# Kernel tuning notes

Hardware: AMD Instinct MI355X
Metric: run time of the kernel (lower is better)

Reference implementation:

```python
import jax, jax.numpy as jnp
import numpy as np

D, NH, DH, DM = 1024, 16, 64, 4096
B, S = 2, 2048
EPS = 1e-5


def _layernorm(x, w, b):
    mu = jnp.mean(x, axis=-1, keepdims=True)
    var = jnp.mean((x - mu) ** 2, axis=-1, keepdims=True)
    return (x - mu) * jax.lax.rsqrt(var + EPS) * w + b


def setup_inputs() -> dict:
    key = jax.random.key(0)
    ks = jax.random.split(key, 8)
    scale = D ** (-0.5)
    x = jax.random.normal(ks[0], (B, S, D), dtype=jnp.float32)
    WQ = jax.random.normal(ks[1], (NH, D, DH), dtype=jnp.float32) * scale
    WK = jax.random.normal(ks[2], (NH, D, DH), dtype=jnp.float32) * scale
    WV = jax.random.normal(ks[3], (NH, D, DH), dtype=jnp.float32) * scale
    WO = jax.random.normal(ks[4], (NH, DH, D), dtype=jnp.float32) * scale
    # MLP: torch Linear default init ~ U(-1/sqrt(fan_in), 1/sqrt(fan_in)); stored as [in, out]
    W1 = jax.random.uniform(ks[5], (D, DM), dtype=jnp.float32, minval=-1.0, maxval=1.0) * D ** (-0.5)
    b1 = jnp.zeros((DM,), dtype=jnp.float32)
    W2 = jax.random.uniform(ks[6], (DM, D), dtype=jnp.float32, minval=-1.0, maxval=1.0) * DM ** (-0.5)
    b2 = jnp.zeros((D,), dtype=jnp.float32)
    ln1_w = jnp.ones((D,), dtype=jnp.float32)
    ln1_b = jnp.zeros((D,), dtype=jnp.float32)
    ln2_w = jnp.ones((D,), dtype=jnp.float32)
    ln2_b = jnp.zeros((D,), dtype=jnp.float32)
    return {"x": x, "WQ": WQ, "WK": WK, "WV": WV, "WO": WO,
            "W1": W1, "b1": b1, "W2": W2, "b2": b2,
            "ln1_w": ln1_w, "ln1_b": ln1_b, "ln2_w": ln2_w, "ln2_b": ln2_b}


def reference(x, WQ, WK, WV, WO, W1, b1, W2, b2, ln1_w, ln1_b, ln2_w, ln2_b):
    s = x.shape[1]
    dh = WQ.shape[-1]
    r = x
    h = _layernorm(x, ln1_w, ln1_b)
    # batched across all heads (original loops over h; math identical)
    Q = jnp.einsum('bsd,hde->bhse', h, WQ)
    K = jnp.einsum('bsd,hde->bhse', h, WK)
    V = jnp.einsum('bsd,hde->bhse', h, WV)
    scores = jnp.einsum('bhqe,bhke->bhqk', Q, K) / jnp.sqrt(jnp.float32(dh))
    causal = jnp.tril(jnp.ones((s, s), dtype=bool))  # True = keep
    scores = jnp.where(causal, scores, -jnp.inf)
    attn = jax.nn.softmax(scores, axis=-1)
    ctx = jnp.einsum('bhqk,bhke->bhqe', attn, V)
    ao = jnp.einsum('bhqe,hed->bqd', ctx, WO)  # sum over heads
    x = r + ao
    h2 = _layernorm(x, ln2_w, ln2_b)
    mlp = jax.nn.gelu(h2 @ W1 + b1, approximate=False) @ W2 + b2
    return x + mlp
```

## Files before the change

kernel.cpp:

```cpp
#include <hip/hip_runtime.h>
#include <hip/hip_bf16.h>
#include <cstdint>

#define D_MODEL 1024
#define NHEADS 16
#define DHEAD 64
#define DMLP 4096
#define BATCH 2
#define SEQ 2048
#define ROWS (BATCH*SEQ)
#define LN_EPS 1e-5f

typedef __attribute__((ext_vector_type(8))) short short8;
typedef __attribute__((ext_vector_type(4))) float f32x4;

typedef const __attribute__((address_space(1))) uint32_t* gas_ptr;
typedef __attribute__((address_space(3))) uint32_t* las_ptr;

__device__ __forceinline__ short f2bf(float f) {
  union { float f; uint32_t u; } v; v.f = f;
  uint32_t r = v.u + 0x7FFFu + ((v.u >> 16) & 1u);
  return (short)(r >> 16);
}
__device__ __forceinline__ float bf2f(short s) {
  union { uint32_t u; float f; } v; v.u = ((uint32_t)(uint16_t)s) << 16;
  return v.f;
}

__global__ void ln_kernel(const float* __restrict__ x, const float* __restrict__ w,
                          const float* __restrict__ b, short* __restrict__ out) {
  int row = blockIdx.x;
  int t = threadIdx.x;
  const float4 v = ((const float4*)(x + (size_t)row * D_MODEL))[t];
  float s = v.x + v.y + v.z + v.w;
  float s2 = v.x*v.x + v.y*v.y + v.z*v.z + v.w*v.w;
#pragma unroll
  for (int k = 1; k < 64; k <<= 1) { s += __shfl_xor(s, k); s2 += __shfl_xor(s2, k); }
  __shared__ float red[8];
  int wv = t >> 6;
  if ((t & 63) == 0) { red[wv] = s; red[wv + 4] = s2; }
  __syncthreads();
  s = red[0] + red[1] + red[2] + red[3];
  s2 = red[4] + red[5] + red[6] + red[7];
  float mu = s * (1.0f / D_MODEL);
  float var = s2 * (1.0f / D_MODEL) - mu * mu;
  float rstd = rsqrtf(var + LN_EPS);
  const float4 wv4 = ((const float4*)w)[t];
  const float4 bv4 = ((const float4*)b)[t];
  short4 o4;
  o4.x = f2bf((v.x - mu) * rstd * wv4.x + bv4.x);
  o4.y = f2bf((v.y - mu) * rstd * wv4.y + bv4.y);
  o4.z = f2bf((v.z - mu) * rstd * wv4.z + bv4.z);
  o4.w = f2bf((v.w - mu) * rstd * wv4.w + bv4.w);
  *(short4*)(out + (size_t)row * D_MODEL + t * 4) = o4;
}

__global__ void reduce_ln(float* __restrict__ out, const float* __restrict__ part,
                          const float* __restrict__ w, const float* __restrict__ b,
                          short* __restrict__ h2) {
  int row = blockIdx.x;
  int t = threadIdx.x;
  float4 v = ((float4*)(out + (size_t)row * D_MODEL))[t];
  const float4 q = ((const float4*)(part + (size_t)row * D_MODEL))[t];
  v.x += q.x; v.y += q.y; v.z += q.z; v.w += q.w;
  ((float4*)(out + (size_t)row * D_MODEL))[t] = v;
  float s = v.x + v.y + v.z + v.w;
  float s2 = v.x*v.x + v.y*v.y + v.z*v.z + v.w*v.w;
#pragma unroll
  for (int k = 1; k < 64; k <<= 1) { s += __shfl_xor(s, k); s2 += __shfl_xor(s2, k); }
  __shared__ float red[8];
  int wv = t >> 6;
  if ((t & 63) == 0) { red[wv] = s; red[wv + 4] = s2; }
  __syncthreads();
  s = red[0] + red[1] + red[2] + red[3];
  s2 = red[4] + red[5] + red[6] + red[7];
  float mu = s * (1.0f / D_MODEL);
  float var = s2 * (1.0f / D_MODEL) - mu * mu;
  float rstd = rsqrtf(var + LN_EPS);
  const float4 wv4 = ((const float4*)w)[t];
  const float4 bv4 = ((const float4*)b)[t];
  short4 o4;
  o4.x = f2bf((v.x - mu) * rstd * wv4.x + bv4.x);
  o4.y = f2bf((v.y - mu) * rstd * wv4.y + bv4.y);
  o4.z = f2bf((v.z - mu) * rstd * wv4.z + bv4.z);
  o4.w = f2bf((v.w - mu) * rstd * wv4.w + bv4.w);
  *(short4*)(h2 + (size_t)row * D_MODEL + t * 4) = o4;
}

__global__ __launch_bounds__(256) void repack_w(const float* __restrict__ W, short* __restrict__ out,
                                                int nkt, int ks1, int ks2, int ns1, int ns2) {
  const int cp = blockIdx.x, kt = blockIdx.y;
  const int t = threadIdx.x;
  const int cc = t & 127;
  const int kh = t >> 7;
  const int n = cp * 128 + cc;
  const int nbase = (n >> 6) * ns1 + (n & 63) * ns2;
  short* dst = out + (((size_t)cp * nkt + kt) * 128 + cc) * 64;
#pragma unroll
  for (int ci = 0; ci < 4; ci++) {
    const int c = kh * 4 + ci;
    short8 ch;
#pragma unroll
    for (int j = 0; j < 8; j++) {
      int k = kt * 64 + c * 8 + j;
      ch[j] = f2bf(W[(k >> 6) * ks1 + (k & 63) * ks2 + nbase]);
    }
    const int sp = c ^ (cc & 7);
    *(short8*)(dst + sp * 8) = ch;
  }
}

template<int EPI>
__global__ __launch_bounds__(256) void gemm_bt(const short* __restrict__ A, const short* __restrict__ Bpk,
    const float* __restrict__ bias, const float* __restrict__ resid,
    float* __restrict__ outf, short* __restrict__ outb, float* __restrict__ part,
    int M, int N, int K, int LDA, int KFULL) {
  __shared__ alignas(16) short As[2][8192];
  __shared__ alignas(16) short Bs[2][8192];
  const int t = threadIdx.x;
  const int l = t & 63, w = t >> 6;
  const int l15 = l & 15, l4 = l >> 4;

  const int nx = gridDim.x;
  const int sw = nx >> 3;
  int dd = blockIdx.y * nx + blockIdx.x;
  const int xcd = dd & 7, li = dd >> 3;
  const int bx = xcd * sw + (li % sw);
  const int by = li / sw;
  const int row0 = by * 128, col0 = bx * 128;

  const int NKT = KFULL >> 6;
  int ktB = 0;
  if (EPI == 5) {
    A  += (size_t)blockIdx.z * K;
    ktB = blockIdx.z * (K >> 6);
  }

  f32x4 acc[4][4] = {};
  char* AsB = (char*)As;
  char* BsB = (char*)Bs;

  const short* aP[4];
#pragma unroll
  for (int i = 0; i < 4; i++) {
    const int g = i * 256 + t;
    const int gr = g >> 3, sp = g & 7;
    aP[i] = A + (size_t)(row0 + gr) * LDA + ((sp ^ (gr & 7)) << 3);
  }
  const short* bP = Bpk + ((size_t)bx * NKT + ktB) * 8192 + t * 8;
  const int d16 = t * 16;
  int sb = 0;

  auto stg = [&]() {
#pragma unroll
    for (int i = 0; i < 4; i++) {
      __builtin_amdgcn_global_load_lds((gas_ptr)(aP[i]),          (las_ptr)(AsB + sb + i * 4096 + d16), 16, 0, 0);
      __builtin_amdgcn_global_load_lds((gas_ptr)(bP + i * 2048),  (las_ptr)(BsB + sb + i * 4096 + d16), 16, 0, 0);
    }
#pragma unroll
    for (int i = 0; i < 4; i++) aP[i] += 64;
    bP += 8192;
    sb ^= 16384;
  };

  const int nk = K >> 6;
  stg();
  asm volatile("s_waitcnt vmcnt(0)" ::: "memory");
  __builtin_amdgcn_s_barrier();

  const int wr = (w >> 1) * 64, wc = (w & 1) * 64;

  for (int ti = 0; ti < nk; ti++) {
    const int bo = (ti & 1) * 16384;
    if (ti + 1 < nk) stg();
#pragma unroll
    for (int kg = 0; kg < 2; kg++) {
      const int sl = ((kg * 4 + l4) ^ (l15 & 7)) * 16;
      short8 a[4], bfr[4];
#pragma unroll
      for (int m = 0; m < 4; m++) a[m]   = *(const short8*)(AsB + bo + (wr + m * 16 + l15) * 128 + sl);
#pragma unroll
      for (int n = 0; n < 4; n++) bfr[n] = *(const short8*)(BsB + bo + (wc + n * 16 + l15) * 128 + sl);
#pragma unroll
      for (int m = 0; m < 4; m++)
#pragma unroll
        for (int n = 0; n < 4; n++)
          acc[m][n] = __builtin_amdgcn_mfma_f32_16x16x32_bf16(a[m], bfr[n], acc[m][n], 0, 0, 0);
    }
    if (ti + 1 < nk) { asm volatile("s_waitcnt vmcnt(0)" ::: "memory"); }
    __builtin_amdgcn_s_barrier();
  }

#pragma unroll
  for (int m = 0; m < 4; m++) {
#pragma unroll
    for (int n = 0; n < 4; n++) {
#pragma unroll
      for (int j = 0; j < 4; j++) {
        int R_ = row0 + wr + m * 16 + l4 * 4 + j;
        int C_ = col0 + wc + n * 16 + l15;
        float v = acc[m][n][j];
        size_t o = (size_t)R_ * N + C_;
        if (EPI == 0) {
          outb[o] = f2bf(v);
        } else if (EPI == 2) {
          float xx = v + bias[C_];
          outb[o] = f2bf(0.5f * xx * (1.0f + erff(xx * 0.70710678118f)));
        } else if (EPI == 5) {
          if (blockIdx.z == 0) outf[o] = v + (bias ? bias[C_] : 0.0f) + resid[o];
          else part[o] = v;
        }
      }
    }
  }
}

__global__ void reduce1(float* __restrict__ out, const float* __restrict__ p, int n4) {
  for (int i = blockIdx.x * 256 + threadIdx.x; i < n4; i += gridDim.x * 256) {
    float4 o = ((float4*)out)[i];
    float4 q = ((const float4*)p)[i];
    o.x += q.x; o.y += q.y; o.z += q.z; o.w += q.w;
    ((float4*)out)[i] = o;
  }
}

__device__ __forceinline__ void attn_step(
    int kt_, int qt, int bufP,
    const short* __restrict__ base, const short* __restrict__ vbase,
    short8& vWA, short8& vWB,
    short8& vLA, short8& vLB,
    const short8 qf[2],
    char* KsB, char* VtB, char* PlB,
    f32x4 acc[4], float mrun[4], float lrun[4],
    int w, int l, int q0, int vr, int vd0)
{
  const int l15 = l & 15, l4 = l >> 4;
  const int bufQ = bufP ^ 1;
  if (kt_ < qt) {
#pragma unroll
    for (int i = 0; i < 8; i++) {
      int d = vd0 + i;
      int cs = (vr >> 2) ^ ((d >> 3) & 7);
      uint32_t val = (uint32_t)(uint16_t)vWA[i] | ((uint32_t)(uint16_t)vWB[i] << 16);
      *(uint32_t*)(VtB + bufQ * 9216 + d * 144 + cs * 16 + (vr & 3) * 4) = val;
    }
#pragma unroll
    for (int i = 0; i < 2; i++) {
      int g = (w * 2 + i) * 64 + l;
      int key = g >> 3, ck = g & 7;
      const short* src = base + (size_t)((kt_ + 1) * 64 + key) * 3072 + 1024 + ((ck ^ (key & 7)) * 8);
      __builtin_amdgcn_global_load_lds((gas_ptr)src, (las_ptr)(KsB + bufQ * 8192 + g * 16), 16, 0, 0);
    }
  }
  if (kt_ + 2 <= qt) {
    vLA = *(const short8*)(vbase + (size_t)((kt_ + 2) * 64 + 2 * vr) * 3072);
    vLB = *(const short8*)(vbase + (size_t)((kt_ + 2) * 64 + 2 * vr + 1) * 3072);
  }

  f32x4 sc[4];
#pragma unroll
  for (int cb = 0; cb < 4; cb++) {
    f32x4 s = {};
    int key = cb * 16 + l15;
#pragma unroll
    for (int c = 0; c < 2; c++) {
      int ck = (c * 4 + l4) ^ (key & 7);
      short8 kf = *(const short8*)(KsB + bufP * 8192 + key * 128 + ck * 16);
      s = __builtin_amdgcn_mfma_f32_16x16x32_bf16(qf[c], kf, s, 0, 0, 0);
    }
    sc[cb] = s;
  }

  const bool lastt = (kt_ == qt);
  float alpha[4];
#pragma unroll
  for (int jj = 0; jj < 4; jj++) {
    int qg = q0 + l4 * 4 + jj;
    float s0 = sc[0][jj] * 0.125f;
    float s1 = sc[1][jj] * 0.125f;
    float s2 = sc[2][jj] * 0.125f;
    float s3 = sc[3][jj] * 0.125f;
    if (lastt) {
      int kg = kt_ * 64 + l15;
      if (kg      > qg) s0 = -1e30f;
      if (kg + 16 > qg) s1 = -1e30f;
      if (kg + 32 > qg) s2 = -1e30f;
      if (kg + 48 > qg) s3 = -1e30f;
    }
    float rm = fmaxf(fmaxf(s0, s1), fmaxf(s2, s3));
    rm = fmaxf(rm, __shfl_xor(rm, 1));
    rm = fmaxf(rm, __shfl_xor(rm, 2));
    rm = fmaxf(rm, __shfl_xor(rm, 4));
    rm = fmaxf(rm, __shfl_xor(rm, 8));
    float nm = fmaxf(mrun[jj], rm);
    float al = __expf(mrun[jj] - nm);
    mrun[jj] = nm;
    float p0 = __expf(s0 - nm), p1 = __expf(s1 - nm);
    float p2 = __expf(s2 - nm), p3 = __expf(s3 - nm);
    float ps = p0 + p1 + p2 + p3;
    ps += __shfl_xor(ps, 1);
    ps += __shfl_xor(ps, 2);
    ps += __shfl_xor(ps, 4);
    ps += __shfl_xor(ps, 8);
    lrun[jj] = lrun[jj] * al + ps;
    alpha[jj] = al;
    short* pr = (short*)(PlB + (l4 * 4 + jj) * 144);
    pr[l15]      = f2bf(p0);
    pr[16 + l15] = f2bf(p1);
    pr[32 + l15] = f2bf(p2);
    pr[48 + l15] = f2bf(p3);
  }
#pragma unroll
  for (int db = 0; db < 4; db++) {
    f32x4 a = acc[db];
    a[0] *= alpha[0]; a[1] *= alpha[1]; a[2] *= alpha[2]; a[3] *= alpha[3];
    acc[db] = a;
  }
#pragma unroll
  for (int kc = 0; kc < 2; kc++) {
    short8 pf = *(const short8*)(PlB + l15 * 144 + kc * 64 + l4 * 16);
#pragma unroll
    for (int db = 0; db < 4; db++) {
      int d = db * 16 + l15;
      int cs = (kc * 4 + l4) ^ ((d >> 3) & 7);
      short8 vf = *(const short8*)(VtB + bufP * 9216 + d * 144 + cs * 16);
      acc[db] = __builtin_amdgcn_mfma_f32_16x16x32_bf16(pf, vf, acc[db], 0, 0, 0);
    }
  }
}

__global__ __launch_bounds__(256) void attn_mfma(const short* __restrict__ qkv, short* __restrict__ ctx) {
  __shared__ alignas(16) short Ks[2 * 64 * 64];
  __shared__ alignas(16) short Vt[2 * 64 * 72];
  __shared__ alignas(16) short Pl[4][16 * 72];
  const int t = threadIdx.x;
  const int l = t & 63;
  const int w = t >> 6;
  const int l15 = l & 15, l4 = l >> 4;
  const int bh = blockIdx.x;
  const int b = bh >> 4, h = bh & 15;
  const int qt = (gridDim.y - 1) - blockIdx.y;
  const int q0 = qt * 64 + w * 16;

  const short* base = qkv + (size_t)b * SEQ * 3072 + h * 64;

  short8 qf[2];
#pragma unroll
  for (int c = 0; c < 2; c++)
    qf[c] = *(const short8*)(base + (size_t)(q0 + l15) * 3072 + c * 32 + l4 * 8);

  const int vr = t >> 3;
  const int vd0 = (t & 7) * 8;
  const short* vbase = base + 2048 + vd0;

  char* KsB = (char*)Ks;
  char* VtB = (char*)Vt;
  char* PlB = (char*)&Pl[w][0];

  short8 va0, vb0, va1, vb1;
  va0 = *(const short8*)(vbase + (size_t)(2 * vr) * 3072);
  vb0 = *(const short8*)(vbase + (size_t)(2 * vr + 1) * 3072);
  if (qt >= 1) {
    va1 = *(const short8*)(vbase + (size_t)(64 + 2 * vr) * 3072);
    vb1 = *(const short8*)(vbase + (size_t)(64 + 2 * vr + 1) * 3072);
  }
#pragma unroll
  for (int i = 0; i < 8; i++) {
    int d = vd0 + i;
    int cs = (vr >> 2) ^ ((d >> 3) & 7);
    uint32_t val = (uint32_t)(uint16_t)va0[i] | ((uint32_t)(uint16_t)vb0[i] << 16);
    *(uint32_t*)(VtB + d * 144 + cs * 16 + (vr & 3) * 4) = val;
  }
#pragma unroll
  for (int i = 0; i < 2; i++) {
    int g = (w * 2 + i) * 64 + l;
    int key = g >> 3, ck = g & 7;
    const short* src = base + (size_t)key * 3072 + 1024 + ((ck ^ (key & 7)) * 8);
    __builtin_amdgcn_global_load_lds((gas_ptr)src, (las_ptr)(KsB + g * 16), 16, 0, 0);
  }
  __syncthreads();

  f32x4 acc[4] = {};
  float mrun[4] = {-1e30f, -1e30f, -1e30f, -1e30f};
  float lrun[4] = {0.f, 0.f, 0.f, 0.f};

  int kt = 0;
  while (true) {
    attn_step(kt, qt, 0, base, vbase, va1, vb1, va0, vb0, qf,
              KsB, VtB, PlB, acc, mrun, lrun, w, l, q0, vr, vd0);
    __syncthreads();
    if (++kt > qt) break;
    attn_step(kt, qt, 1, base, vbase, va0, vb0, va1, vb1, qf,
              KsB, VtB, PlB, acc, mrun, lrun, w, l, q0, vr, vd0);
    __syncthreads();
    if (++kt > qt) break;
  }

  float inv[4];
#pragma unroll
  for (int jj = 0; jj < 4; jj++) inv[jj] = 1.0f / lrun[jj];
  short* obase = ctx + (size_t)(b * SEQ + q0) * D_MODEL + h * 64;
#pragma unroll
  for (int db = 0; db < 4; db++)
#pragma unroll
    for (int jj = 0; jj < 4; jj++)
      obase[(size_t)(l4 * 4 + jj) * D_MODEL + db * 16 + l15] = f2bf(acc[db][jj] * inv[jj]);
}

extern "C" void kernel_launch(void* const* d_in, const int* in_sizes, int n_in,
                              void* d_out, int out_size, void* d_ws, size_t ws_size,
                              hipStream_t stream) {
  (void)in_sizes; (void)n_in; (void)out_size; (void)ws_size;
  const float* x    = (const float*)d_in[0];
  const float* WQ   = (const float*)d_in[1];
  const float* WK   = (const float*)d_in[2];
  const float* WV   = (const float*)d_in[3];
  const float* WO   = (const float*)d_in[4];
  const float* W1   = (const float*)d_in[5];
  const float* b1   = (const float*)d_in[6];
  const float* W2   = (const float*)d_in[7];
  const float* b2   = (const float*)d_in[8];
  const float* ln1w = (const float*)d_in[9];
  const float* ln1b = (const float*)d_in[10];
  const float* ln2w = (const float*)d_in[11];
  const float* ln2b = (const float*)d_in[12];
  float* out = (float*)d_out;

  char* p = (char*)d_ws;
  short* h1    = (short*)p; p += (size_t)ROWS * D_MODEL * 2;
  short* ctx   = (short*)p; p += (size_t)ROWS * D_MODEL * 2;
  short* h2    = (short*)p; p += (size_t)ROWS * D_MODEL * 2;
  short* m1    = (short*)p; p += (size_t)ROWS * DMLP * 2;
  short* wqkvT = (short*)p; p += (size_t)3 * D_MODEL * D_MODEL * 2;
  short* woT   = (short*)p; p += (size_t)D_MODEL * D_MODEL * 2;
  short* w1T   = (short*)p; p += (size_t)D_MODEL * DMLP * 2;
  short* w2T   = (short*)p; p += (size_t)D_MODEL * DMLP * 2;
  short* qkv   = (short*)p; p += (size_t)ROWS * 3 * D_MODEL * 2;

  float* fp1 = (float*)qkv;

  repack_w<<<dim3(8, 16), 256, 0, stream>>>(WQ, wqkvT,                  16, 4096, 64, 65536, 1);
  repack_w<<<dim3(8, 16), 256, 0, stream>>>(WK, wqkvT + 8 * 16 * 8192,  16, 4096, 64, 65536, 1);
  repack_w<<<dim3(8, 16), 256, 0, stream>>>(WV, wqkvT + 16 * 16 * 8192, 16, 4096, 64, 65536, 1);
  repack_w<<<dim3(8, 16), 256, 0, stream>>>(WO, woT, 16, 65536, 1024, 64, 1);
  repack_w<<<dim3(32, 16), 256, 0, stream>>>(W1, w1T, 16, 262144, 4096, 64, 1);
  repack_w<<<dim3(8, 64), 256, 0, stream>>>(W2, w2T, 64, 65536, 1024, 64, 1);

  ln_kernel<<<ROWS, 256, 0, stream>>>(x, ln1w, ln1b, h1);
  gemm_bt<0><<<dim3(3 * D_MODEL / 128, ROWS / 128), 256, 0, stream>>>(
      h1, wqkvT, nullptr, nullptr, nullptr, qkv, nullptr,
      ROWS, 3 * D_MODEL, D_MODEL, D_MODEL, D_MODEL);
  attn_mfma<<<dim3(BATCH * NHEADS, SEQ / 64), 256, 0, stream>>>(qkv, ctx);
  gemm_bt<5><<<dim3(D_MODEL / 128, ROWS / 128, 2), 256, 0, stream>>>(
      ctx, woT, nullptr, x, out, nullptr, fp1,
      ROWS, D_MODEL, D_MODEL / 2, D_MODEL, D_MODEL);
  reduce_ln<<<ROWS, 256, 0, stream>>>(out, fp1, ln2w, ln2b, h2);
  gemm_bt<2><<<dim3(DMLP / 128, ROWS / 128), 256, 0, stream>>>(
      h2, w1T, b1, nullptr, nullptr, m1, nullptr,
      ROWS, DMLP, D_MODEL, D_MODEL, D_MODEL);
  gemm_bt<5><<<dim3(D_MODEL / 128, ROWS / 128, 2), 256, 0, stream>>>(
      m1, w2T, b2, out, out, nullptr, fp1,
      ROWS, D_MODEL, DMLP / 2, DMLP, DMLP);
  reduce1<<<2048, 256, 0, stream>>>(out, fp1, ROWS * D_MODEL / 4);
}
```

Measured before the change: 299.5 us.

## Use split-K 256x256-tile GEMM for MLP up-projection with separate GELU pass

Replaces the 128-tile fused-GELU GEMM for h2@W1 with a new 512-thread kernel that computes 256x256 output tiles. It splits K in two and writes bf16 partials into reused workspace buffers (m1 and h1). A separate elementwise kernel then sums the partials, adds the bias and applies erf-GELU. W1 is now converted with a plain tiled transpose instead of the swizzled repack, and the workspace is reordered. The goal is more data reuse per tile and better occupancy across the grid. In exchange it adds an extra full pass over the 4096-wide activation, rounds the partial sums to bf16, and uses scalar epilogue stores.

```diff
diff --git a/kernel.cpp b/kernel.cpp
--- a/kernel.cpp
+++ b/kernel.cpp
@@ -87,6 +87,36 @@
   *(short4*)(h2 + (size_t)row * D_MODEL + t * 4) = o4;
 }
 
+__global__ __launch_bounds__(256) void transpose_tile(const float* __restrict__ src, short* __restrict__ dst,
+                                                      int R, int C, int srcMatStride) {
+  __shared__ float tile[64][65];
+  const int m = blockIdx.z;
+  const int r0 = blockIdx.y * 64, c0 = blockIdx.x * 64;
+  const int tx = threadIdx.x & 15, ty = threadIdx.x >> 4;
+  const float* s = src + (size_t)m * srcMatStride + (size_t)r0 * C + c0;
+#pragma unroll
+  for (int i = 0; i < 4; i++) {
+    float4 v = *(const float4*)(s + (size_t)(ty + i * 16) * C + tx * 4);
+    tile[ty + i * 16][tx * 4 + 0] = v.x;
+    tile[ty + i * 16][tx * 4 + 1] = v.y;
+    tile[ty + i * 16][tx * 4 + 2] = v.z;
+    tile[ty + i * 16][tx * 4 + 3] = v.w;
+  }
+  __syncthreads();
+  short* d = dst + (size_t)m * C * R + (size_t)c0 * R + r0;
+#pragma unroll
+  for (int p = 0; p < 4; p++) {
+    int c = ty + p * 16;
+    int r4 = tx * 4;
+    short4 o;
+    o.x = f2bf(tile[r4 + 0][c]);
+    o.y = f2bf(tile[r4 + 1][c]);
+    o.z = f2bf(tile[r4 + 2][c]);
+    o.w = f2bf(tile[r4 + 3][c]);
+    *(short4*)(d + (size_t)c * R + r4) = o;
+  }
+}
+
 __global__ __launch_bounds__(256) void repack_w(const float* __restrict__ W, short* __restrict__ out,
                                                 int nkt, int ks1, int ks2, int ns1, int ns2) {
   const int cp = blockIdx.x, kt = blockIdx.y;
@@ -107,6 +137,111 @@
     }
     const int sp = c ^ (cc & 7);
     *(short8*)(dst + sp * 8) = ch;
+  }
+}
+
+__global__ __launch_bounds__(512) void gemm256b(const short* __restrict__ A, const short* __restrict__ BT,
+    short* __restrict__ p0, short* __restrict__ p1,
+    int M, int N, int K, int LDA, int LDB) {
+  __shared__ alignas(16) short As[2][8192];
+  __shared__ alignas(16) short Bs[2][8192];
+  const int t = threadIdx.x;
+  const int l = t & 63, w = t >> 6;
+  const int l15 = l & 15, l4 = l >> 4;
+  const int wm = w >> 2, wn = w & 3;
+
+  const int nx = gridDim.x;
+  const int sw = nx >> 3;
+  int dd = blockIdx.y * nx + blockIdx.x;
+  const int xcd = dd & 7, li = dd >> 3;
+  const int bx = xcd * sw + (li % sw);
+  const int by = li / sw;
+  const int row0 = by * 256, col0 = bx * 256;
+
+  const int z = blockIdx.z;
+  A  += (size_t)z * K;
+  BT += (size_t)z * K;
+  short* dst = (z == 0) ? p0 : p1;
+
+  f32x4 acc[8][4] = {};
+  char* AsB = (char*)As;
+  char* BsB = (char*)Bs;
+
+  const short* aP[2];
+  const short* bP[2];
+#pragma unroll
+  for (int j = 0; j < 2; j++) {
+    const int g = t + j * 512;
+    const int gr = g >> 2, sp = g & 3;
+    const int co = (sp ^ ((gr >> 1) & 3)) << 3;
+    aP[j] = A  + (size_t)(row0 + gr) * LDA + co;
+    bP[j] = BT + (size_t)(col0 + gr) * LDB + co;
+  }
+  const int d16a = t * 16, d16b = t * 16 + 8192;
+  int sb = 0;
+
+  auto stg = [&]() {
+    __builtin_amdgcn_global_load_lds((gas_ptr)(aP[0]), (las_ptr)(AsB + sb + d16a), 16, 0, 0);
+    __builtin_amdgcn_global_load_lds((gas_ptr)(aP[1]), (las_ptr)(AsB + sb + d16b), 16, 0, 0);
+    __builtin_amdgcn_global_load_lds((gas_ptr)(bP[0]), (las_ptr)(BsB + sb + d16a), 16, 0, 0);
+    __builtin_amdgcn_global_load_lds((gas_ptr)(bP[1]), (las_ptr)(BsB + sb + d16b), 16, 0, 0);
+    aP[0] += 32; aP[1] += 32; bP[0] += 32; bP[1] += 32;
+    sb ^= 16384;
+  };
+
+  const int nk = K >> 5;
+  stg();
+  asm volatile("s_waitcnt vmcnt(0)" ::: "memory");
+  __builtin_amdgcn_s_barrier();
+
+  const int sl = (l4 ^ ((l15 >> 1) & 3)) * 16;
+
+  for (int ti = 0; ti < nk; ti++) {
+    const int bo = (ti & 1) * 16384;
+    if (ti + 1 < nk) stg();
+    short8 af[8], bfr[4];
+#pragma unroll
+    for (int fr = 0; fr < 8; fr++) af[fr] = *(const short8*)(AsB + bo + (wm * 128 + fr * 16 + l15) * 64 + sl);
+#pragma unroll
+    for (int n = 0; n < 4; n++) bfr[n] = *(const short8*)(BsB + bo + (wn * 64 + n * 16 + l15) * 64 + sl);
+#pragma unroll
+    for (int fr = 0; fr < 8; fr++)
+#pragma unroll
+      for (int n = 0; n < 4; n++)
+        acc[fr][n] = __builtin_amdgcn_mfma_f32_16x16x32_bf16(af[fr], bfr[n], acc[fr][n], 0, 0, 0);
+    if (ti + 1 < nk) { asm volatile("s_waitcnt vmcnt(0)" ::: "memory"); }
+    __builtin_amdgcn_s_barrier();
+  }
+
+#pragma unroll
+  for (int fr = 0; fr < 8; fr++) {
+#pragma unroll
+    for (int n = 0; n < 4; n++) {
+#pragma unroll
+      for (int j = 0; j < 4; j++) {
+        int R = row0 + wm * 128 + fr * 16 + l4 * 4 + j;
+        int C = col0 + wn * 64 + n * 16 + l15;
+        dst[(size_t)R * N + C] = f2bf(acc[fr][n][j]);
+      }
+    }
+  }
+}
+
+__global__ void gelu_sum(const short* __restrict__ p0, const short* __restrict__ p1,
+                         const float* __restrict__ b1, short* __restrict__ m1) {
+  const int n4 = ROWS * DMLP / 4;
+  for (int i = blockIdx.x * 256 + threadIdx.x; i < n4; i += gridDim.x * 256) {
+    short4 a = ((const short4*)p0)[i];
+    short4 b = ((const short4*)p1)[i];
+    int col = (i & (DMLP / 4 - 1)) * 4;
+    const float4 bb = *(const float4*)(b1 + col);
+    short4 o;
+    float xx;
+    xx = bf2f(a.x) + bf2f(b.x) + bb.x; o.x = f2bf(0.5f * xx * (1.0f + erff(xx * 0.70710678118f)));
+    xx = bf2f(a.y) + bf2f(b.y) + bb.y; o.y = f2bf(0.5f * xx * (1.0f + erff(xx * 0.70710678118f)));
+    xx = bf2f(a.z) + bf2f(b.z) + bb.z; o.z = f2bf(0.5f * xx * (1.0f + erff(xx * 0.70710678118f)));
+    xx = bf2f(a.w) + bf2f(b.w) + bb.w; o.w = f2bf(0.5f * xx * (1.0f + erff(xx * 0.70710678118f)));
+    ((short4*)m1)[i] = o;
   }
 }
 
@@ -427,23 +562,25 @@
   float* out = (float*)d_out;
 
   char* p = (char*)d_ws;
+  short* h2    = (short*)p; p += (size_t)ROWS * D_MODEL * 2;
+  short* w1T   = (short*)p; p += (size_t)D_MODEL * DMLP * 2;
+  short* w2T   = (short*)p; p += (size_t)D_MODEL * DMLP * 2;
+  short* m1    = (short*)p; p += (size_t)ROWS * DMLP * 2;
   short* h1    = (short*)p; p += (size_t)ROWS * D_MODEL * 2;
   short* ctx   = (short*)p; p += (size_t)ROWS * D_MODEL * 2;
-  short* h2    = (short*)p; p += (size_t)ROWS * D_MODEL * 2;
-  short* m1    = (short*)p; p += (size_t)ROWS * DMLP * 2;
   short* wqkvT = (short*)p; p += (size_t)3 * D_MODEL * D_MODEL * 2;
   short* woT   = (short*)p; p += (size_t)D_MODEL * D_MODEL * 2;
-  short* w1T   = (short*)p; p += (size_t)D_MODEL * DMLP * 2;
-  short* w2T   = (short*)p; p += (size_t)D_MODEL * DMLP * 2;
   short* qkv   = (short*)p; p += (size_t)ROWS * 3 * D_MODEL * 2;
 
   float* fp1 = (float*)qkv;
+  short* pb0 = m1;
+  short* pb1 = h1;
 
   repack_w<<<dim3(8, 16), 256, 0, stream>>>(WQ, wqkvT,                  16, 4096, 64, 65536, 1);
   repack_w<<<dim3(8, 16), 256, 0, stream>>>(WK, wqkvT + 8 * 16 * 8192,  16, 4096, 64, 65536, 1);
   repack_w<<<dim3(8, 16), 256, 0, stream>>>(WV, wqkvT + 16 * 16 * 8192, 16, 4096, 64, 65536, 1);
   repack_w<<<dim3(8, 16), 256, 0, stream>>>(WO, woT, 16, 65536, 1024, 64, 1);
-  repack_w<<<dim3(32, 16), 256, 0, stream>>>(W1, w1T, 16, 262144, 4096, 64, 1);
+  transpose_tile<<<dim3(64, 16, 1), 256, 0, stream>>>(W1, w1T, 1024, 4096, 0);
   repack_w<<<dim3(8, 64), 256, 0, stream>>>(W2, w2T, 64, 65536, 1024, 64, 1);
 
   ln_kernel<<<ROWS, 256, 0, stream>>>(x, ln1w, ln1b, h1);
@@ -455,9 +592,9 @@
       ctx, woT, nullptr, x, out, nullptr, fp1,
       ROWS, D_MODEL, D_MODEL / 2, D_MODEL, D_MODEL);
   reduce_ln<<<ROWS, 256, 0, stream>>>(out, fp1, ln2w, ln2b, h2);
-  gemm_bt<2><<<dim3(DMLP / 128, ROWS / 128), 256, 0, stream>>>(
-      h2, w1T, b1, nullptr, nullptr, m1, nullptr,
-      ROWS, DMLP, D_MODEL, D_MODEL, D_MODEL);
+  gemm256b<<<dim3(DMLP / 256, ROWS / 256, 2), 512, 0, stream>>>(
+      h2, w1T, pb0, pb1, ROWS, DMLP, D_MODEL / 2, D_MODEL, D_MODEL);
+  gelu_sum<<<2048, 256, 0, stream>>>(pb0, pb1, b1, m1);
   gemm_bt<5><<<dim3(D_MODEL / 128, ROWS / 128, 2), 256, 0, stream>>>(
       m1, w2T, b2, out, out, nullptr, fp1,
       ROWS, D_MODEL, DMLP / 2, DMLP, DMLP);
```

Measured after the change: 316.8 us. 1.06x slower.
